# Optimization experiments

Measured on AMD Instinct MI355X. Metric: run time of the kernel, lower is better.

## Reference

```python
import jax, jax.numpy as jnp
import numpy as np

BS, NSEQ, SPO_NSEQ, NUM_BOX, NUM_CTX, MAXC = 1024, 32, 32, 128, 5, 4


def _build_structure(seed=0):
    # Random trees over NSEQ nodes per sample: parent(i) = (i-1)//br, br in {2,3,4}.
    # adj[child, parent] = edge_id (as in the torch adj_matrices, -1 = no edge).
    rng = np.random.RandomState(seed)
    adjs = np.full((BS, NSEQ, NSEQ), -1, np.int64)
    trav = []
    for b in range(BS):
        br = rng.randint(2, 5)
        for i in range(1, NSEQ):
            adjs[b, i, (i - 1) // br] = i - 1  # edge ids < SPO_NSEQ
        trav.append(sorted(set(((np.arange(1, NSEQ) - 1) // br).tolist())))  # internal nodes, top-down
    L = max(len(t) for t in trav)
    padded = np.stack([np.pad(np.asarray(t), (L - len(t), 0), constant_values=-1) for t in trav])
    parent_idx = np.zeros((L, BS), np.int32)
    parent_valid = np.zeros((L, BS), np.float32)
    child_idx = np.zeros((L, BS, MAXC), np.int32)
    child_valid = np.zeros((L, BS, MAXC), np.float32)
    edge_idx = np.zeros((L, BS, MAXC), np.int32)
    flat_sample = np.zeros((L, BS), np.int32)
    flat_slot = np.zeros((L, BS), np.int32)
    for it in range(L):
        pairs = []  # flat children ordering: sample 0's children, then sample 1's, ...
        for b in range(BS):
            p = int(padded[b, it])
            ch = np.nonzero(adjs[b, :, p] != -1)[0] if p != -1 else np.array([], np.int64)
            if p == -1 or len(ch) == 0:
                pairs.append((b, 0))  # dummy child 0, masked out (no_parent_or_no_children=0)
            else:
                parent_idx[it, b] = p
                parent_valid[it, b] = 1.0
                for j, c in enumerate(ch):
                    child_idx[it, b, j] = c
                    child_valid[it, b, j] = 1.0
                    edge_idx[it, b, j] = adjs[b, c, p]
                pairs.extend((b, j) for j in range(len(ch)))
        for f in range(BS):  # flat row f used as update_mask[sampid] in the torch code
            flat_sample[it, f], flat_slot[it, f] = pairs[f]
    return parent_idx, parent_valid, child_idx, child_valid, edge_idx, flat_sample, flat_slot


def setup_inputs() -> dict:
    key = jax.random.key(0)
    ks = jax.random.split(key, 6)
    pi, pv, ci, cv, ei, fs, fl = _build_structure()
    ent_attn = jax.random.normal(ks[0], (BS, NSEQ, NUM_BOX), jnp.float32)
    spo_attn = jax.random.normal(ks[1], (BS, SPO_NSEQ, NUM_BOX, NUM_CTX), jnp.float32)
    base = jax.random.randint(ks[2], (BS, SPO_NSEQ, NUM_BOX), 0, NUM_BOX)
    # distinct ctx indices per (b, e, box) slot so the scatter has no duplicate columns
    ctx_idx_adjusted = ((base[..., None] + jnp.arange(NUM_CTX, dtype=jnp.int32) * 7) % NUM_BOX).astype(jnp.int32)
    roi_mask = (jax.random.uniform(ks[3], (BS, SPO_NSEQ, NUM_BOX, NUM_CTX)) < 0.9).astype(jnp.float32)
    roi_cls = jax.random.randint(ks[4], (BS, NUM_BOX), -1, 20).astype(jnp.int32)
    weight_on_children = jax.random.uniform(ks[5], (BS, NSEQ, NUM_BOX), dtype=jnp.float32)
    return dict(ent_attn=ent_attn, spo_attn=spo_attn, ctx_idx_adjusted=ctx_idx_adjusted,
                roi_mask=roi_mask, roi_cls=roi_cls, weight_on_children=weight_on_children,
                parent_idx=jnp.asarray(pi), parent_valid=jnp.asarray(pv),
                child_idx=jnp.asarray(ci), child_valid=jnp.asarray(cv),
                edge_idx=jnp.asarray(ei), flat_sample=jnp.asarray(fs), flat_slot=jnp.asarray(fl))


def _propagate(ent_attn, spo_attn, roi_mask, weight_on_children,
               ctx_idx_adjusted, roi_cls,
               parent_idx, parent_valid, child_idx, child_valid, edge_idx, flat_sample, flat_slot):
    bs, nseq, nbox = ent_attn.shape
    bar = jnp.arange(bs)
    cls_mask = (roi_cls != -1).astype(ent_attn.dtype)            # [bs, nbox]
    L = parent_idx.shape[0]                                      # tree depth (small, static)
    for it in range(L):
        pidx, pval = parent_idx[it], parent_valid[it]            # [bs]
        cidx, cval, eidx = child_idx[it], child_valid[it], edge_idx[it]  # [bs, C]
        # selected_children_atn: [bs, C, nbox]
        ch_atn = ent_attn[bar[:, None], cidx] * cval[..., None] * cls_mask[:, None, :]
        # per-edge gathers + transpose(1,2): [bs, spo, nbox, ctx] -> [bs, C, ctx, nbox]
        gather_T = lambda t: jnp.swapaxes(t[bar[:, None], eidx], -1, -2)
        k_ctx = gather_T(ctx_idx_adjusted)                       # int indices
        m_roi = gather_T(roi_mask)
        filt = m_roi * cval[..., None, None]                     # filter_mask
        k_scores = gather_T(spo_attn) * filt * cls_mask[:, None, None, :]
        # sgmn transfer: sum over boxes -> [bs, C, ctx]
        transfer = jnp.sum(ch_atn[:, :, None, :] * k_scores * m_roi, axis=-1) + 1e-6
        # faithful to torch quirk: value row = first child of sample (cnt), index row = flat row sampid
        upd_cols = k_ctx[flat_sample[it], flat_slot[it], :, 0]   # [bs, ctx] box indices
        add_to_sub = jnp.full((bs, nbox), 1e-6, ent_attn.dtype).at[bar[:, None], upd_cols].set(transfer[:, 0, :])
        sub_atn = ent_attn[bar, pidx]                            # [bs, nbox]
        upd = sub_atn + add_to_sub * weight_on_children[bar, pidx]   # opt='add'
        # NormAttnMap (cossim): norm = max(|x|) detached, clamped >= 1
        norm = jax.lax.stop_gradient(jnp.max(jnp.abs(upd), axis=-1, keepdims=True))
        upd = upd / jnp.where(norm <= 1, jnp.ones_like(norm), norm)
        upd = jnp.where(roi_cls == -1, -1.0, upd)                # opt 'add' -> -1
        new_rows = jnp.where(pval[:, None] > 0, upd, sub_atn)    # only write where bs_mask
        ent_attn = ent_attn.at[bar, pidx].set(new_rows)
    return ent_attn


def reference(ent_attn, spo_attn, ctx_idx_adjusted, roi_mask, roi_cls, weight_on_children,
              parent_idx, parent_valid, child_idx, child_valid, edge_idx, flat_sample, flat_slot):
    return _propagate(ent_attn, spo_attn, roi_mask, weight_on_children,
                      ctx_idx_adjusted, roi_cls,
                      parent_idx, parent_valid, child_idx, child_valid, edge_idx, flat_sample, flat_slot)
```

## Files before the change

kernel.cpp:

```cpp
#include <hip/hip_runtime.h>

constexpr int kBS   = 1024;
constexpr int kNSEQ = 32;
constexpr int kNBOX = 128;
constexpr int kNCTX = 5;
constexpr int kMAXC = 4;

__global__ __launch_bounds__(256) void copy_f4(const float4* __restrict__ s,
                                               float4* __restrict__ d, int n4) {
    int i = blockIdx.x * 256 + threadIdx.x;
    const int str = gridDim.x * 256;
    for (; i < n4; i += str) d[i] = s[i];
}

__global__ __launch_bounds__(128) void propagate(
    const float* __restrict__ ent,
    const float* __restrict__ spo,
    const int*   __restrict__ ctx,
    const float* __restrict__ roi,
    const int*   __restrict__ cls,
    const float* __restrict__ woc,
    const int*   __restrict__ pidx,
    const float* __restrict__ pval,
    const int*   __restrict__ cidx,
    const int*   __restrict__ eidx,
    const int*   __restrict__ fsamp,
    const int*   __restrict__ fslot,
    float* __restrict__ out)
{
    const int b   = blockIdx.x;
    const int it  = blockIdx.y;
    const int idx = it * kBS + b;
    if (pval[idx] <= 0.0f) return;

    const int k   = threadIdx.x;
    const int p   = pidx[idx];
    const int c0  = cidx[idx * kMAXC];
    const int e0  = eidx[idx * kMAXC];
    const int fs  = fsamp[idx];
    const int fl  = fslot[idx];
    const int ep  = eidx[(it * kBS + fs) * kMAXC + fl];

    const int   clsk = cls[b * kNBOX + k];
    const float cm   = (clsk != -1) ? 1.0f : 0.0f;
    const float a    = ent[(b * kNSEQ + c0) * kNBOX + k] * cm;

    const size_t sb = ((size_t)(b * kNSEQ + e0) * kNBOX + k) * kNCTX;
    float part[kNCTX];
    #pragma unroll
    for (int c = 0; c < kNCTX; ++c)
        part[c] = a * spo[sb + c] * roi[sb + c];

    #pragma unroll
    for (int off = 32; off >= 1; off >>= 1) {
        #pragma unroll
        for (int c = 0; c < kNCTX; ++c)
            part[c] += __shfl_xor(part[c], off, 64);
    }
    __shared__ float wsum[2][kNCTX];
    __shared__ float wmax[2];
    const int wave = k >> 6;
    if ((k & 63) == 0) {
        #pragma unroll
        for (int c = 0; c < kNCTX; ++c) wsum[wave][c] = part[c];
    }
    __syncthreads();
    float t[kNCTX];
    #pragma unroll
    for (int c = 0; c < kNCTX; ++c) t[c] = wsum[0][c] + wsum[1][c] + 1e-6f;

    const int cbase = (fs * kNSEQ + ep) * kNBOX * kNCTX;
    float val = 1e-6f;
    #pragma unroll
    for (int c = 0; c < kNCTX; ++c) {
        if (ctx[cbase + c] == k) val = t[c];
    }

    const int pb  = (b * kNSEQ + p) * kNBOX + k;
    float upd = ent[pb] + val * woc[pb];

    float m = fabsf(upd);
    #pragma unroll
    for (int off = 32; off >= 1; off >>= 1)
        m = fmaxf(m, __shfl_xor(m, off, 64));
    if ((k & 63) == 0) wmax[wave] = m;
    __syncthreads();
    const float norm = fmaxf(wmax[0], wmax[1]);
    if (norm > 1.0f) upd /= norm;
    if (clsk == -1) upd = -1.0f;
    out[pb] = upd;
}

extern "C" void kernel_launch(void* const* d_in, const int* in_sizes, int n_in,
                              void* d_out, int out_size, void* d_ws, size_t ws_size,
                              hipStream_t stream) {
    const float* ent   = (const float*)d_in[0];
    const float* spo   = (const float*)d_in[1];
    const int*   ctx   = (const int*)  d_in[2];
    const float* roi   = (const float*)d_in[3];
    const int*   cls   = (const int*)  d_in[4];
    const float* woc   = (const float*)d_in[5];
    const int*   pidx  = (const int*)  d_in[6];
    const float* pval  = (const float*)d_in[7];
    const int*   cidx  = (const int*)  d_in[8];
    const int*   eidx  = (const int*)  d_in[10];
    const int*   fsamp = (const int*)  d_in[11];
    const int*   fslot = (const int*)  d_in[12];
    float* out = (float*)d_out;

    const int L  = in_sizes[6] / kBS;
    const int n4 = out_size / 4;

    copy_f4<<<dim3(2048), dim3(256), 0, stream>>>((const float4*)ent, (float4*)out, n4);
    propagate<<<dim3(kBS, L), dim3(128), 0, stream>>>(
        ent, spo, ctx, roi, cls, woc, pidx, pval, cidx, eidx, fsamp, fslot, out);
}
```

Baseline: 243.6 us.

## Fuse output copy into propagate kernel with per-row parent lookup

Removes the separate full-tensor copy kernel and launches one block per (sample, row) instead of per (sample, iteration). Each block scans the L iterations to find whether its row is an updated parent; rows that are not parents copy the input straight to the output, and parent rows compute the update. This drops one kernel launch and a redundant write of the parent rows. In exchange every block performs a short serial scan of pval/pidx and the copy is done with scalar stores instead of float4. It also assumes each parent row is updated in at most one iteration and that iterations are independent.

```diff
diff --git a/kernel.cpp b/kernel.cpp
--- a/kernel.cpp
+++ b/kernel.cpp
@@ -6,14 +6,7 @@
 constexpr int kNCTX = 5;
 constexpr int kMAXC = 4;
 
-__global__ __launch_bounds__(256) void copy_f4(const float4* __restrict__ s,
-                                               float4* __restrict__ d, int n4) {
-    int i = blockIdx.x * 256 + threadIdx.x;
-    const int str = gridDim.x * 256;
-    for (; i < n4; i += str) d[i] = s[i];
-}
-
-__global__ __launch_bounds__(128) void propagate(
+__global__ __launch_bounds__(128) void fused_propagate(
     const float* __restrict__ ent,
     const float* __restrict__ spo,
     const int*   __restrict__ ctx,
@@ -26,15 +19,25 @@
     const int*   __restrict__ eidx,
     const int*   __restrict__ fsamp,
     const int*   __restrict__ fslot,
-    float* __restrict__ out)
+    float* __restrict__ out,
+    int L)
 {
     const int b   = blockIdx.x;
-    const int it  = blockIdx.y;
+    const int row = blockIdx.y;
+    const int k   = threadIdx.x;
+    const int rb  = (b * kNSEQ + row) * kNBOX + k;
+
+    int it = -1;
+    for (int i = 0; i < L; ++i) {
+        const int j = i * kBS + b;
+        if (pval[j] > 0.0f && pidx[j] == row) { it = i; break; }
+    }
+    if (it < 0) {
+        out[rb] = ent[rb];
+        return;
+    }
+
     const int idx = it * kBS + b;
-    if (pval[idx] <= 0.0f) return;
-
-    const int k   = threadIdx.x;
-    const int p   = pidx[idx];
     const int c0  = cidx[idx * kMAXC];
     const int e0  = eidx[idx * kMAXC];
     const int fs  = fsamp[idx];
@@ -76,8 +79,7 @@
         if (ctx[cbase + c] == k) val = t[c];
     }
 
-    const int pb  = (b * kNSEQ + p) * kNBOX + k;
-    float upd = ent[pb] + val * woc[pb];
+    float upd = ent[rb] + val * woc[rb];
 
     float m = fabsf(upd);
     #pragma unroll
@@ -88,7 +90,7 @@
     const float norm = fmaxf(wmax[0], wmax[1]);
     if (norm > 1.0f) upd /= norm;
     if (clsk == -1) upd = -1.0f;
-    out[pb] = upd;
+    out[rb] = upd;
 }
 
 extern "C" void kernel_launch(void* const* d_in, const int* in_sizes, int n_in,
@@ -108,10 +110,8 @@
     const int*   fslot = (const int*)  d_in[12];
     float* out = (float*)d_out;
 
-    const int L  = in_sizes[6] / kBS;
-    const int n4 = out_size / 4;
+    const int L = in_sizes[6] / kBS;
 
-    copy_f4<<<dim3(2048), dim3(256), 0, stream>>>((const float4*)ent, (float4*)out, n4);
-    propagate<<<dim3(kBS, L), dim3(128), 0, stream>>>(
-        ent, spo, ctx, roi, cls, woc, pidx, pval, cidx, eidx, fsamp, fslot, out);
+    fused_propagate<<<dim3(kBS, kNSEQ), dim3(128), 0, stream>>>(
+        ent, spo, ctx, roi, cls, woc, pidx, pval, cidx, eidx, fsamp, fslot, out, L);
 }
```

Result: slower. 262.1 us (+7.6%).
